# Performance work log

Hardware: AMD Instinct MI355X
Metric: run time of the kernel (lower is better)

The kernel has to match this reference:

```python
import jax, jax.numpy as jnp
import numpy as np

HEADS = 12


def setup_inputs() -> dict:
    rng = jax.random.key(0)
    ks = jax.random.split(rng, 12)
    B, L, D = 8, 64, 768
    s = 1.0 / np.sqrt(D)  # keep projections well-scaled
    return {
        "key": jax.random.normal(ks[0], (B, L, L, D), jnp.float32),
        "value": jax.random.normal(ks[1], (B, L, L, D), jnp.float32),
        "query": jax.random.normal(ks[2], (B, L, D), jnp.float32),
        "mask": jnp.ones((B, L, L), jnp.float32),
        "Wk": jax.random.normal(ks[3], (D, D), jnp.float32) * s,
        "bk": jax.random.normal(ks[4], (D,), jnp.float32) * 0.01,
        "Wv": jax.random.normal(ks[5], (D, D), jnp.float32) * s,
        "bv": jax.random.normal(ks[6], (D,), jnp.float32) * 0.01,
        "Wq": jax.random.normal(ks[7], (D, D), jnp.float32) * s,
        "bq": jax.random.normal(ks[8], (D,), jnp.float32) * 0.01,
        "Wo": jax.random.normal(ks[9], (D, D), jnp.float32) * s,
        "bo": jax.random.normal(ks[10], (D,), jnp.float32) * 0.01,
    }


def reference(key, value, query, mask, Wk, bk, Wv, bv, Wq, bq, Wo, bo):
    # key/value: [B, L, L, D]; query: [B, L, D]; mask: [B, L, L]
    B, L, _, D = key.shape
    h = HEADS
    d = D // h
    # Projections (torch Linear y = x W^T + b; here W stored transposed so y = x @ W + b)
    Kp = (key @ Wk + bk).reshape(B, L, L, h, d)    # [B, i, j, h, d]
    Vp = (value @ Wv + bv).reshape(B, L, L, h, d)  # [B, i, j, h, d]
    Qp = (query @ Wq + bq).reshape(B, L, h, d)     # [B, i, h, d]
    Qp = Qp / jnp.sqrt(jnp.asarray(d, Qp.dtype))
    # scores[b,h,i,j] = sum_d Q[b,i,h,d] * K[b,i,j,h,d]  (query i attends over its own j-row)
    scores = jnp.einsum('bihd,bijhd->bhij', Qp, Kp)
    # multiplicative mask (as in the original: scores = scores * mask)
    scores = scores * mask[:, None, :, :]
    attn = jax.nn.softmax(scores, axis=-1)
    # dropout is identity at inference
    ctx = jnp.einsum('bhij,bijhd->bihd', attn, Vp).reshape(B, L, D)
    return ctx @ Wo + bo  # [B, L, D]
```

## Files before the change

### kernel.cpp

```cpp
#include <hip/hip_runtime.h>

#define DMODEL 768
#define NHEADS 12
#define RTOT   512
#define BIW    9216

__global__ __launch_bounds__(256) void linear16(
    const float* __restrict__ src, int ars, int scm,
    const float* __restrict__ W, const float* __restrict__ bias,
    float* __restrict__ dst, int drs, float scale)
{
    __shared__ float At[16][64];
    __shared__ float Bt[64][32];
    const int rt = blockIdx.x, ct = blockIdx.y, t = threadIdx.x;
    const int sk = ((ct * 32) >> 6) * scm;
    const int c  = t & 31;
    const int rg = t >> 5;

    const int ar0 = t >> 4,          ak0 = t & 15;
    const int bk0 = t >> 3,          bc0 = (t & 7) * 4;
    const int bk1 = (t + 256) >> 3,  bc1 = ((t + 256) & 7) * 4;

    float4 va0, vb0, vb1;
    auto LD = [&](int kb) {
        va0 = *(const float4*)&src[(size_t)(rt * 16 + ar0) * ars + sk + kb * 64 + ak0 * 4];
        vb0 = *(const float4*)&W[(size_t)(kb * 64 + bk0) * DMODEL + ct * 32 + bc0];
        vb1 = *(const float4*)&W[(size_t)(kb * 64 + bk1) * DMODEL + ct * 32 + bc1];
    };

    LD(0);
    float acc[2] = {0.f, 0.f};

    for (int kb = 0; kb < 12; ++kb) {
        if (kb) __syncthreads();
        *(float4*)&At[ar0][ak0 * 4] = va0;
        *(float4*)&Bt[bk0][bc0] = vb0;
        *(float4*)&Bt[bk1][bc1] = vb1;
        __syncthreads();
        if (kb < 11) LD(kb + 1);
        #pragma unroll
        for (int kq = 0; kq < 16; ++kq) {
            float b0 = Bt[kq * 4 + 0][c], b1 = Bt[kq * 4 + 1][c];
            float b2 = Bt[kq * 4 + 2][c], b3 = Bt[kq * 4 + 3][c];
            #pragma unroll
            for (int i = 0; i < 2; ++i) {
                float4 a = *(const float4*)&At[rg * 2 + i][kq * 4];
                acc[i] += a.x * b0 + a.y * b1 + a.z * b2 + a.w * b3;
            }
        }
    }
    const float bb = bias[ct * 32 + c];
    #pragma unroll
    for (int i = 0; i < 2; ++i)
        dst[(size_t)(rt * 16 + rg * 2 + i) * drs + ct * 32 + c] = (acc[i] + bb) * scale;
}

__global__ __launch_bounds__(256) void u_kernel(
    const float* __restrict__ qp, const float* __restrict__ Wk, const float* __restrict__ bk,
    float* __restrict__ u, float* __restrict__ cvec)
{
    __shared__ float Qt[32][64];
    __shared__ float Bt[64][65];
    const int rt = blockIdx.x, mt = blockIdx.y, h = blockIdx.z, t = threadIdx.x;

    #pragma unroll
    for (int kk = 0; kk < 2; ++kk) {
        int i4 = t + kk * 256;
        int r = i4 >> 4, dq = i4 & 15;
        *(float4*)&Qt[r][dq * 4] =
            *(const float4*)&qp[(size_t)(rt * 32 + r) * DMODEL + h * 64 + dq * 4];
    }
    #pragma unroll
    for (int kk = 0; kk < 4; ++kk) {
        int i4 = t + kk * 256;
        int m = i4 >> 4, dq = i4 & 15;
        float4 v = *(const float4*)&Wk[(size_t)(mt * 64 + m) * DMODEL + h * 64 + dq * 4];
        Bt[m][dq * 4 + 0] = v.x; Bt[m][dq * 4 + 1] = v.y;
        Bt[m][dq * 4 + 2] = v.z; Bt[m][dq * 4 + 3] = v.w;
    }
    __syncthreads();

    const int c = t & 63, rg = t >> 6;
    float acc[8] = {0.f,0.f,0.f,0.f,0.f,0.f,0.f,0.f};
    #pragma unroll
    for (int dq = 0; dq < 16; ++dq) {
        float b0 = Bt[c][dq * 4 + 0], b1 = Bt[c][dq * 4 + 1];
        float b2 = Bt[c][dq * 4 + 2], b3 = Bt[c][dq * 4 + 3];
        #pragma unroll
        for (int i = 0; i < 8; ++i) {
            float4 a = *(const float4*)&Qt[rg * 8 + i][dq * 4];
            acc[i] += a.x * b0 + a.y * b1 + a.z * b2 + a.w * b3;
        }
    }
    #pragma unroll
    for (int i = 0; i < 8; ++i)
        u[(size_t)(rt * 32 + rg * 8 + i) * BIW + h * DMODEL + mt * 64 + c] = acc[i];

    if (mt == 0 && t < 32) {
        float s = 0.f;
        for (int d = 0; d < 64; ++d) s += bk[h * 64 + d] * Qt[t][d];
        cvec[(rt * 32 + t) * NHEADS + h] = s;
    }
}

__global__ __launch_bounds__(256, 2) void scores_k(
    const float* __restrict__ key, const float* __restrict__ u,
    const float* __restrict__ cvec, const float* __restrict__ mask,
    float* __restrict__ sc_out)
{
    const int bi   = blockIdx.x;
    const int jh   = blockIdx.y;
    const int t    = threadIdx.x;
    const int lane = t & 63;
    const int wv   = t >> 6;
    const int h0   = wv * 3;
    const size_t kvb = (size_t)bi * 64 * DMODEL;
    const float* kbase = &key[kvb + lane * 4];

    float4 uf[3][3];
    #pragma unroll
    for (int i = 0; i < 3; ++i)
        #pragma unroll
        for (int cch = 0; cch < 3; ++cch)
            uf[i][cch] = *(const float4*)&u[(size_t)bi * BIW + (h0 + i) * DMODEL + cch * 256 + lane * 4];

    const float cv0 = cvec[bi * NHEADS + h0 + 0];
    const float cv1 = cvec[bi * NHEADS + h0 + 1];
    const float cv2 = cvec[bi * NHEADS + h0 + 2];

    float4 kA[12], kB[12];

    auto LOADK = [&](float4* kk, int b) {
        const float* kp = kbase + (size_t)(jh * 32 + b * 4) * DMODEL;
        #pragma unroll
        for (int r = 0; r < 4; ++r)
            #pragma unroll
            for (int cch = 0; cch < 3; ++cch)
                kk[r * 3 + cch] = *(const float4*)(kp + (size_t)r * DMODEL + cch * 256);
    };

    auto COMPUTE = [&](const float4* kk, int b) {
        const int j0 = jh * 32 + b * 4;
        float v[3][4];
        #pragma unroll
        for (int i = 0; i < 3; ++i)
            #pragma unroll
            for (int r = 0; r < 4; ++r) v[i][r] = 0.f;

        #pragma unroll
        for (int cch = 0; cch < 3; ++cch)
            #pragma unroll
            for (int i = 0; i < 3; ++i) {
                const float4 uu = uf[i][cch];
                #pragma unroll
                for (int r = 0; r < 4; ++r) {
                    const float4 kr = kk[r * 3 + cch];
                    v[i][r] += kr.x * uu.x + kr.y * uu.y + kr.z * uu.z + kr.w * uu.w;
                }
            }

        float s[3][2];
        #pragma unroll
        for (int i = 0; i < 3; ++i)
            #pragma unroll
            for (int r = 0; r < 2; ++r) {
                float lo = v[i][r], hi = v[i][r + 2];
                float tl = __shfl_xor(lo, 32), th = __shfl_xor(hi, 32);
                s[i][r] = (lane < 32) ? lo + tl : hi + th;
            }
        float tt[3];
        #pragma unroll
        for (int i = 0; i < 3; ++i) {
            float lo = s[i][0], hi = s[i][1];
            float tl = __shfl_xor(lo, 16), th = __shfl_xor(hi, 16);
            tt[i] = ((lane & 16) == 0) ? lo + tl : hi + th;
        }
        #pragma unroll
        for (int o = 8; o >= 1; o >>= 1)
            #pragma unroll
            for (int i = 0; i < 3; ++i) tt[i] += __shfl_xor(tt[i], o);

        if ((lane & 15) == 0) {
            const int q = lane >> 4;
            const int j = j0 + q;
            const float mk = mask[bi * 64 + j];
            sc_out[(size_t)bi * 768 + (h0 + 0) * 64 + j] = (tt[0] + cv0) * mk;
            sc_out[(size_t)bi * 768 + (h0 + 1) * 64 + j] = (tt[1] + cv1) * mk;
            sc_out[(size_t)bi * 768 + (h0 + 2) * 64 + j] = (tt[2] + cv2) * mk;
        }
    };

    LOADK(kA, 0);
    #pragma unroll 1
    for (int b = 0; b < 8; b += 2) {
        LOADK(kB, b + 1);
        COMPUTE(kA, b);
        if (b + 2 < 8) LOADK(kA, b + 2);
        COMPUTE(kB, b + 1);
    }
}

__global__ __launch_bounds__(256) void pv_k(
    const float* __restrict__ value, const float* __restrict__ sc,
    float* __restrict__ w)
{
    __shared__ float attn[NHEADS][64];

    const int bi   = blockIdx.x;
    const int ms   = blockIdx.y;
    const int t    = threadIdx.x;
    const int lane = t & 63;
    const int wv   = t >> 6;
    const size_t kvb = (size_t)bi * 64 * DMODEL;

    #pragma unroll
    for (int i = 0; i < 3; ++i) {
        const int h = wv * 3 + i;
        float s = sc[(size_t)bi * 768 + h * 64 + lane];
        float mx = s;
        #pragma unroll
        for (int o = 1; o < 64; o <<= 1) mx = fmaxf(mx, __shfl_xor(mx, o));
        float e = __expf(s - mx);
        float sm = e;
        #pragma unroll
        for (int o = 1; o < 64; o <<= 1) sm += __shfl_xor(sm, o);
        attn[h][lane] = e / sm;
    }
    __syncthreads();

    const int mo = ms * 256 + t;
    float acc[NHEADS];
    #pragma unroll
    for (int h = 0; h < NHEADS; ++h) acc[h] = 0.f;
    const float* vb = value + kvb + mo;

    #pragma unroll 4
    for (int j4 = 0; j4 < 64; j4 += 4) {
        float v0 = vb[(size_t)(j4 + 0) * DMODEL];
        float v1 = vb[(size_t)(j4 + 1) * DMODEL];
        float v2 = vb[(size_t)(j4 + 2) * DMODEL];
        float v3 = vb[(size_t)(j4 + 3) * DMODEL];
        #pragma unroll
        for (int h = 0; h < NHEADS; ++h) {
            float4 at = *(const float4*)&attn[h][j4];
            acc[h] += at.x * v0 + at.y * v1 + at.z * v2 + at.w * v3;
        }
    }
    #pragma unroll
    for (int h = 0; h < NHEADS; ++h)
        w[(size_t)bi * BIW + h * DMODEL + mo] = acc[h];
}

extern "C" void kernel_launch(void* const* d_in, const int* in_sizes, int n_in,
                              void* d_out, int out_size, void* d_ws, size_t ws_size,
                              hipStream_t stream) {
    const float* key   = (const float*)d_in[0];
    const float* value = (const float*)d_in[1];
    const float* query = (const float*)d_in[2];
    const float* mask  = (const float*)d_in[3];
    const float* Wk    = (const float*)d_in[4];
    const float* bk    = (const float*)d_in[5];
    const float* Wv    = (const float*)d_in[6];
    const float* bv    = (const float*)d_in[7];
    const float* Wq    = (const float*)d_in[8];
    const float* bq    = (const float*)d_in[9];
    const float* Wo    = (const float*)d_in[10];
    const float* bo    = (const float*)d_in[11];
    float* out = (float*)d_out;

    float* wsf    = (float*)d_ws;
    float* qp_ctx = wsf;
    float* u_w    = wsf + (size_t)RTOT * DMODEL;
    float* cvec   = u_w + (size_t)RTOT * BIW;
    float* sc_ws  = cvec + (size_t)RTOT * NHEADS;

    linear16<<<dim3(32, 24), 256, 0, stream>>>(query, DMODEL, 0, Wq, bq, qp_ctx, DMODEL, 0.125f);
    u_kernel<<<dim3(16, 12, 12), 256, 0, stream>>>(qp_ctx, Wk, bk, u_w, cvec);
    scores_k<<<dim3(512, 2), 256, 0, stream>>>(key, u_w, cvec, mask, sc_ws);
    pv_k<<<dim3(512, 3), 256, 0, stream>>>(value, sc_ws, u_w);
    linear16<<<dim3(32, 24), 256, 0, stream>>>(u_w, BIW, DMODEL, Wv, bv, qp_ctx, DMODEL, 1.0f);
    linear16<<<dim3(32, 24), 256, 0, stream>>>(qp_ctx, DMODEL, 0, Wo, bo, out, DMODEL, 1.0f);
}
```

Baseline: 171.8 us.

## Split pv_k over j across waves with float4 value loads and LDS reduction

The value-times-attention kernel now has each wave handle 16 of the 64 j rows, with each lane loading a float4 of four output columns instead of one scalar per thread. The four waves' partial sums are combined through shared memory in two steps and written out as float4. The goal is wider, more efficient global loads and more memory-level parallelism, with a launch-bounds hint for higher occupancy. In return it adds 24KB of shared memory, two extra barriers and a reduction step, and raises per-thread register use for 48 accumulators. The scores kernel also gets a minor hoist of the jh offset into its base pointer.

```diff
diff --git a/kernel.cpp b/kernel.cpp
--- a/kernel.cpp
+++ b/kernel.cpp
@@ -115,7 +115,7 @@
     const int wv   = t >> 6;
     const int h0   = wv * 3;
     const size_t kvb = (size_t)bi * 64 * DMODEL;
-    const float* kbase = &key[kvb + lane * 4];
+    const float* kbase = &key[kvb + (size_t)jh * 32 * DMODEL + lane * 4];
 
     float4 uf[3][3];
     #pragma unroll
@@ -131,7 +131,7 @@
     float4 kA[12], kB[12];
 
     auto LOADK = [&](float4* kk, int b) {
-        const float* kp = kbase + (size_t)(jh * 32 + b * 4) * DMODEL;
+        const float* kp = kbase + (size_t)(b * 4) * DMODEL;
         #pragma unroll
         for (int r = 0; r < 4; ++r)
             #pragma unroll
@@ -200,11 +200,12 @@
     }
 }
 
-__global__ __launch_bounds__(256) void pv_k(
+__global__ __launch_bounds__(256, 4) void pv_k(
     const float* __restrict__ value, const float* __restrict__ sc,
     float* __restrict__ w)
 {
-    __shared__ float attn[NHEADS][64];
+    __shared__ float  attn[NHEADS][64];
+    __shared__ float4 part[2][NHEADS][64];
 
     const int bi   = blockIdx.x;
     const int ms   = blockIdx.y;
@@ -228,27 +229,48 @@
     }
     __syncthreads();
 
-    const int mo = ms * 256 + t;
-    float acc[NHEADS];
-    #pragma unroll
-    for (int h = 0; h < NHEADS; ++h) acc[h] = 0.f;
-    const float* vb = value + kvb + mo;
-
+    float4 acc[NHEADS];
+    #pragma unroll
+    for (int h = 0; h < NHEADS; ++h) acc[h] = make_float4(0.f, 0.f, 0.f, 0.f);
+
+    const float* vb = value + kvb + ms * 256 + lane * 4;
+    const int jbase = wv * 16;
     #pragma unroll 4
-    for (int j4 = 0; j4 < 64; j4 += 4) {
-        float v0 = vb[(size_t)(j4 + 0) * DMODEL];
-        float v1 = vb[(size_t)(j4 + 1) * DMODEL];
-        float v2 = vb[(size_t)(j4 + 2) * DMODEL];
-        float v3 = vb[(size_t)(j4 + 3) * DMODEL];
+    for (int jj = 0; jj < 16; ++jj) {
+        float4 v4 = *(const float4*)(vb + (size_t)(jbase + jj) * DMODEL);
         #pragma unroll
         for (int h = 0; h < NHEADS; ++h) {
-            float4 at = *(const float4*)&attn[h][j4];
-            acc[h] += at.x * v0 + at.y * v1 + at.z * v2 + at.w * v3;
-        }
-    }
-    #pragma unroll
-    for (int h = 0; h < NHEADS; ++h)
-        w[(size_t)bi * BIW + h * DMODEL + mo] = acc[h];
+            const float a = attn[h][jbase + jj];
+            acc[h].x += a * v4.x; acc[h].y += a * v4.y;
+            acc[h].z += a * v4.z; acc[h].w += a * v4.w;
+        }
+    }
+
+    if (wv < 2) {
+        #pragma unroll
+        for (int h = 0; h < NHEADS; ++h) part[wv][h][lane] = acc[h];
+    }
+    __syncthreads();
+    if (wv >= 2) {
+        #pragma unroll
+        for (int h = 0; h < NHEADS; ++h) {
+            float4 p = part[wv - 2][h][lane];
+            p.x += acc[h].x; p.y += acc[h].y; p.z += acc[h].z; p.w += acc[h].w;
+            part[wv - 2][h][lane] = p;
+        }
+    }
+    __syncthreads();
+
+    #pragma unroll
+    for (int k = 0; k < 3; ++k) {
+        const int p = t + k * 256;
+        const int h = p >> 6, c = p & 63;
+        float4 r0 = part[0][h][c], r1 = part[1][h][c];
+        float4 r;
+        r.x = r0.x + r1.x; r.y = r0.y + r1.y;
+        r.z = r0.z + r1.z; r.w = r0.w + r1.w;
+        *(float4*)&w[(size_t)bi * BIW + h * DMODEL + ms * 256 + c * 4] = r;
+    }
 }
 
 extern "C" void kernel_launch(void* const* d_in, const int* in_sizes, int n_in,
```

New measurement: 162.5 us. 5.4% less time.
